# Performance work log

Hardware: AMD Instinct MI355X
Metric: run time of the kernel (lower is better)

## Reference

```python
import jax, jax.numpy as jnp
import numpy as np

B, S, P = 64, 32, 49
F, E, H, V = 2048, 512, 512, 32000


def setup_inputs() -> dict:
    key = jax.random.key(0)
    ks = jax.random.split(key, 20)
    sc = 0.02
    return {
        "captions": jax.random.randint(ks[0], (B, S), 0, V),
        "features": jax.random.normal(ks[1], (B, P, F), dtype=jnp.float32),
        "embed_table": jax.random.normal(ks[2], (V, E), dtype=jnp.float32) * sc,
        "W_a": jax.random.normal(ks[3], (H, F), dtype=jnp.float32) * sc,
        "b_Wa": jnp.zeros((H,), jnp.float32),
        "U_a": jax.random.normal(ks[4], (H, H), dtype=jnp.float32) * sc,
        "b_Ua": jnp.zeros((H,), jnp.float32),
        "v_a": jax.random.normal(ks[5], (1, H), dtype=jnp.float32) * sc,
        "b_va": jnp.zeros((1,), jnp.float32),
        "W_ih": jax.random.normal(ks[6], (4 * H, E + F), dtype=jnp.float32) * sc,
        "b_ih": jnp.zeros((4 * H,), jnp.float32),
        "W_hh": jax.random.normal(ks[7], (4 * H, H), dtype=jnp.float32) * sc,
        "b_hh": jnp.zeros((4 * H,), jnp.float32),
        "fc_W": jax.random.normal(ks[8], (V, H), dtype=jnp.float32) * sc,
        "fc_b": jnp.zeros((V,), jnp.float32),
        "Wh": jax.random.normal(ks[9], (H, F), dtype=jnp.float32) * sc,
        "bh": jnp.zeros((H,), jnp.float32),
        "Wc": jax.random.normal(ks[10], (H, F), dtype=jnp.float32) * sc,
        "bc": jnp.zeros((H,), jnp.float32),
    }


def reference(captions, features, embed_table, W_a, b_Wa, U_a, b_Ua, v_a, b_va,
              W_ih, b_ih, W_hh, b_hh, fc_W, fc_b, Wh, bh, Wc, bc):
    # Embedding lookup: [B, S, E]
    embed = embed_table[captions]
    # init hidden from mean annotation
    mean_feat = jnp.mean(features, axis=1)            # [B, F]
    h0 = mean_feat @ Wh.T + bh                        # [B, H]
    c0 = mean_feat @ Wc.T + bc
    # W_a(features) is time-invariant: precompute once
    att1 = jnp.einsum('bpf,hf->bph', features, W_a) + b_Wa  # [B, P, H]

    def step(carry, word_embed):
        h, c = carry
        # Bahdanau attention
        att2 = h @ U_a.T + b_Ua                                   # [B, H]
        score = jnp.tanh(att1 + att2[:, None, :]) @ v_a[0] + b_va[0]  # [B, P]
        w = jax.nn.softmax(score, axis=1)                         # [B, P]
        context = jnp.einsum('bp,bpf->bf', w, features)           # [B, F]
        # LSTMCell (PyTorch gate order: i, f, g, o)
        x = jnp.concatenate([word_embed, context], axis=1)        # [B, E+F]
        gates = x @ W_ih.T + b_ih + h @ W_hh.T + b_hh             # [B, 4H]
        i, f, g, o = jnp.split(gates, 4, axis=1)
        c_new = jax.nn.sigmoid(f) * c + jax.nn.sigmoid(i) * jnp.tanh(g)
        h_new = jax.nn.sigmoid(o) * jnp.tanh(c_new)
        # dropout is identity at inference
        logits = h_new @ fc_W.T + fc_b                            # [B, V]
        return (h_new, c_new), (logits, w)

    _, (logits, attw) = jax.lax.scan(step, (h0, c0), jnp.swapaxes(embed, 0, 1))
    outputs = jnp.swapaxes(logits, 0, 1)       # [B, S, V]
    atten_weights = jnp.swapaxes(attw, 0, 1)   # [B, S, P]
    return outputs, atten_weights
```

## Files before the change

kernel.cpp:

```cpp
#include <hip/hip_runtime.h>
#include <hip/hip_fp16.h>

typedef _Float16 f16;
typedef _Float16 f16x2 __attribute__((ext_vector_type(2)));
typedef _Float16 f16x4 __attribute__((ext_vector_type(4)));
typedef _Float16 f16x8 __attribute__((ext_vector_type(8)));
typedef float    f32x4 __attribute__((ext_vector_type(4)));


#define GLD16(g, l)                                                        \
  __builtin_amdgcn_global_load_lds(                                        \
      (const __attribute__((address_space(1))) void*)(g),                  \
      (__attribute__((address_space(3))) void*)(l), 16, 0, 0)

__global__ __launch_bounds__(256) void k_prep(
    const float* __restrict__ feat, const float* __restrict__ W_a,
    const float* __restrict__ W_ih, const float* __restrict__ fc_W,
    const float* __restrict__ W_hh, const float* __restrict__ U_a,
    const float* __restrict__ Wh, const float* __restrict__ Wc,
    const int* __restrict__ caps, const float* __restrict__ etab,
    f16* __restrict__ feat_h, f16* __restrict__ W_a_h,
    f16* __restrict__ W_ih_h, f16* __restrict__ fc_W_h,
    f16* __restrict__ Wcat_h, f16* __restrict__ Whc_h, f16* __restrict__ Aemb) {
  const long c0 = 1605632;
  const long c1 = c0 + 262144;
  const long c2 = c1 + 1310720;
  const long c3 = c2 + 4096000;
  const long c4 = c3 + 262144;
  const long c5 = c4 + 65536;
  const long c6 = c5 + 262144;
  const long c7 = c6 + 262144;
  const long c8 = c7 + 262144;
  long i = (long)blockIdx.x * 256 + threadIdx.x;
  const long stride = (long)gridDim.x * 256;
  for (; i < c8; i += stride) {
    const float4* s; f16x4* d; long j;
    if (i < c0)      { s = (const float4*)feat; d = (f16x4*)feat_h; j = i; }
    else if (i < c1) { s = (const float4*)W_a;  d = (f16x4*)W_a_h;  j = i - c0; }
    else if (i < c2) { s = (const float4*)W_ih; d = (f16x4*)W_ih_h; j = i - c1; }
    else if (i < c3) { s = (const float4*)fc_W; d = (f16x4*)fc_W_h; j = i - c2; }
    else if (i < c4) { s = (const float4*)W_hh; d = (f16x4*)Wcat_h; j = i - c3; }
    else if (i < c5) { s = (const float4*)U_a;  d = (f16x4*)(Wcat_h + 2048l * 512); j = i - c4; }
    else if (i < c6) { s = (const float4*)Wh;   d = (f16x4*)Whc_h;  j = i - c5; }
    else if (i < c7) { s = (const float4*)Wc;   d = (f16x4*)(Whc_h + 1048576l); j = i - c6; }
    else {
      long jj = i - c7;
      int n = (int)(jj >> 7), e4 = (int)(jj & 127);
      int tok = caps[n];
      s = (const float4*)(etab + (long)tok * 512); d = (f16x4*)(Aemb + (long)n * 512); j = e4;
    }
    float4 v = s[j];
    f16x4 o; o.x = (f16)v.x; o.y = (f16)v.y; o.z = (f16)v.z; o.w = (f16)v.w;
    d[j] = o;
  }
}

__global__ __launch_bounds__(256) void k_mean(const f16* __restrict__ feat_h,
                                              f16* __restrict__ mean_h) {
  int b = blockIdx.x;
  int e4 = blockIdx.y * 256 + threadIdx.x;
  const f16x4* src = (const f16x4*)(feat_h + (long)b * 49 * 2048) + e4;
  float s0 = 0.f, s1 = 0.f, s2 = 0.f, s3 = 0.f;
#pragma unroll 7
  for (int p = 0; p < 49; ++p) {
    f16x4 v = src[p * 512];
    s0 += (float)v.x; s1 += (float)v.y; s2 += (float)v.z; s3 += (float)v.w;
  }
  const float inv = 1.f / 49.f;
  f16x4 o; o.x = (f16)(s0 * inv); o.y = (f16)(s1 * inv); o.z = (f16)(s2 * inv); o.w = (f16)(s3 * inv);
  ((f16x4*)(mean_h + (long)b * 2048))[e4] = o;
}

__global__ __launch_bounds__(512) void k_h0split(const float* __restrict__ Rh0,
                                                 const float* __restrict__ bh,
                                                 const float* __restrict__ bc,
                                                 f16* __restrict__ h16,
                                                 float* __restrict__ c_state) {
  int b = blockIdx.x, j = threadIdx.x;
  h16[(long)b * 512 + j] = (f16)(Rh0[(long)b * 1024 + j] + bh[j]);
  c_state[(long)b * 512 + j] = Rh0[(long)b * 1024 + 512 + j] + bc[j];
}

__global__ __launch_bounds__(256) void k_gemm(const f16* __restrict__ A, long lda,
                                              const f16* __restrict__ Bw, long ldb,
                                              const float* __restrict__ bias1,
                                              const float* __restrict__ bias2,
                                              void* __restrict__ Cout, long ldc,
                                              int K, int mode, int n_mtiles) {
  __shared__ f16 As[64][40];
  __shared__ f16 Bs[64][40];
  const int tid = threadIdx.x;
  const int lane = tid & 63, wave = tid >> 6;
  const int bid = blockIdx.x;
  const long m0 = (long)(bid % n_mtiles) * 64, n0 = (long)(bid / n_mtiles) * 64;
  const int lr = tid >> 2, lc = (tid & 3) * 8;
  const int wr = (wave >> 1) * 32, wc = (wave & 1) * 32;
  f32x4 acc[2][2] = {};
  const f16* Ap = A + (m0 + lr) * lda + lc;
  const f16* Bp = Bw + (n0 + lr) * ldb + lc;
  for (int k0 = 0; k0 < K; k0 += 32) {
    uint4 av = *(const uint4*)(Ap + k0);
    uint4 bv = *(const uint4*)(Bp + k0);
    __syncthreads();
    *(uint4*)&As[lr][lc] = av;
    *(uint4*)&Bs[lr][lc] = bv;
    __syncthreads();
#pragma unroll
    for (int mi = 0; mi < 2; ++mi) {
      f16x8 af = *(const f16x8*)&As[wr + mi * 16 + (lane & 15)][(lane >> 4) * 8];
#pragma unroll
      for (int ni = 0; ni < 2; ++ni) {
        f16x8 bf = *(const f16x8*)&Bs[wc + ni * 16 + (lane & 15)][(lane >> 4) * 8];
        acc[mi][ni] = __builtin_amdgcn_mfma_f32_16x16x32_f16(af, bf, acc[mi][ni], 0, 0, 0);
      }
    }
  }
#pragma unroll
  for (int mi = 0; mi < 2; ++mi)
#pragma unroll
    for (int ni = 0; ni < 2; ++ni) {
      int row_b = wr + mi * 16 + (lane >> 4) * 4;
      long gcol = n0 + wc + ni * 16 + (lane & 15);
      float badd = (bias1 ? bias1[gcol] : 0.f) + (bias2 ? bias2[gcol] : 0.f);
#pragma unroll
      for (int r = 0; r < 4; ++r) {
        long grow = m0 + row_b + r;
        float v = acc[mi][ni][r] + badd;
        if (mode == 0)      ((float*)Cout)[grow * ldc + gcol] = v;
        else                ((f16*)Cout)[grow * ldc + gcol] = (f16)v;
      }
    }
}

__global__ __launch_bounds__(512) void k_gemm128b(const f16* __restrict__ A, long lda,
                                                  const f16* __restrict__ Bw, long ldb,
                                                  const float* __restrict__ bias1,
                                                  const float* __restrict__ bias2,
                                                  void* __restrict__ Cout, long ldc,
                                                  int K, int mode, int n_mtiles) {
  __shared__ f16 As[8192];
  __shared__ f16 Bs[8192];
  const int tid = threadIdx.x, lane = tid & 63, wave = tid >> 6;
  const int wm = wave & 3, wn = wave >> 2;
  const int bid = blockIdx.x;
  const long m0 = (long)(bid % n_mtiles) * 128, n0 = (long)(bid / n_mtiles) * 128;
  const int c0 = wave * 128 + lane, c1 = c0 + 64;
  const int r0 = c0 >> 3, s0 = (c0 & 7) ^ (r0 & 7);
  const int r1 = c1 >> 3, s1 = (c1 & 7) ^ (r1 & 7);
  const f16* gA0 = A + (m0 + r0) * lda + s0 * 8;
  const f16* gA1 = A + (m0 + r1) * lda + s1 * 8;
  const f16* gB0 = Bw + (n0 + r0) * ldb + s0 * 8;
  const f16* gB1 = Bw + (n0 + r1) * ldb + s1 * 8;
  f16* lA0 = As + (wave * 128) * 8;
  f16* lA1 = As + (wave * 128 + 64) * 8;
  f16* lB0 = Bs + (wave * 128) * 8;
  f16* lB1 = Bs + (wave * 128 + 64) * 8;
  f32x4 acc[2][4] = {};
  for (int k0 = 0; k0 < K; k0 += 64) {
    GLD16(gA0 + k0, lA0); GLD16(gA1 + k0, lA1);
    GLD16(gB0 + k0, lB0); GLD16(gB1 + k0, lB1);
    __syncthreads();
#pragma unroll
    for (int ks = 0; ks < 2; ++ks) {
      const int sp = (ks * 4 + (lane >> 4)) ^ (lane & 7);
#pragma unroll
      for (int mi = 0; mi < 2; ++mi) {
        const int rA = wm * 32 + mi * 16 + (lane & 15);
        f16x8 af = *(const f16x8*)(As + rA * 64 + sp * 8);
#pragma unroll
        for (int ni = 0; ni < 4; ++ni) {
          const int rB = wn * 64 + ni * 16 + (lane & 15);
          f16x8 bf = *(const f16x8*)(Bs + rB * 64 + sp * 8);
          acc[mi][ni] = __builtin_amdgcn_mfma_f32_16x16x32_f16(af, bf, acc[mi][ni], 0, 0, 0);
        }
      }
    }
    __syncthreads();
  }
#pragma unroll
  for (int mi = 0; mi < 2; ++mi)
#pragma unroll
    for (int ni = 0; ni < 4; ++ni) {
      int row_b = wm * 32 + mi * 16 + (lane >> 4) * 4;
      long gcol = n0 + wn * 64 + ni * 16 + (lane & 15);
      float badd = (bias1 ? bias1[gcol] : 0.f) + (bias2 ? bias2[gcol] : 0.f);
#pragma unroll
      for (int r = 0; r < 4; ++r) {
        long grow = m0 + row_b + r;
        float v = acc[mi][ni][r] + badd;
        if (mode == 0)      ((float*)Cout)[grow * ldc + gcol] = v;
        else if (mode == 1) ((f16*)Cout)[grow * ldc + gcol] = (f16)v;
        else                ((f16*)Cout)[grow * 2048 + ((gcol & 511) << 2) + (gcol >> 9)] = (f16)v;
      }
    }
}

__global__ __launch_bounds__(256) void k_rgemm(const f16* __restrict__ h16,
                                               const f16* __restrict__ Wcat,
                                               float* __restrict__ R) {
  const int tid = threadIdx.x, lane = tid & 63, wave = tid >> 6;
  const int n0 = blockIdx.x * 64;
  const int l15 = lane & 15;
  const int koff = (lane >> 4) * 8;
  f32x4 acc[4] = {};
  const f16* Ap = h16 + ((long)(wave * 16 + l15) << 9) + koff;
#pragma unroll
  for (int k0 = 0; k0 < 16; ++k0) {
    f16x8 af = *(const f16x8*)(Ap + k0 * 32);
#pragma unroll
    for (int ni = 0; ni < 4; ++ni) {
      f16x8 bf = *(const f16x8*)(Wcat + ((long)(n0 + ni * 16 + l15) << 9) + koff + k0 * 32);
      acc[ni] = __builtin_amdgcn_mfma_f32_16x16x32_f16(af, bf, acc[ni], 0, 0, 0);
    }
  }
  const int r0 = wave * 16 + (lane >> 4) * 4;
#pragma unroll
  for (int ni = 0; ni < 4; ++ni) {
    int col = n0 + ni * 16 + l15;
#pragma unroll
    for (int r = 0; r < 4; ++r)
      R[(long)(r0 + r) * 2560 + col] = acc[ni][r];
  }
}

__global__ __launch_bounds__(512) void k_step(const float* __restrict__ R,
                                              const float* __restrict__ b_Ua,
                                              const f16* __restrict__ att1,
                                              const float* __restrict__ va,
                                              const f16* __restrict__ featW4,
                                              const float* __restrict__ gates_x,
                                              float* __restrict__ c_state,
                                              f16* __restrict__ h16,
                                              f16* __restrict__ Hbuf,
                                              float* __restrict__ attw_out,
                                              int t) {
  __shared__ float att2[512];
  __shared__ float sc[64];
  __shared__ float wl[49];
  const int b = blockIdx.x, tid = threadIdx.x;
  const int lane = tid & 63, wave = tid >> 6;
  const long n = (long)b * 32 + t;
  const float* Rb = R + (long)b * 2560;
  const float* gx = gates_x + n * 2048;

  float g0 = gx[tid] + Rb[tid];
  float g1 = gx[512 + tid] + Rb[512 + tid];
  float g2 = gx[1024 + tid] + Rb[1024 + tid];
  float g3 = gx[1536 + tid] + Rb[1536 + tid];
  float c = c_state[(long)b * 512 + tid];

  att2[tid] = Rb[2048 + tid] + b_Ua[tid];
  __syncthreads();

  for (int p = wave; p < 49; p += 8) {
    const f16* arow = att1 + ((long)b * 49 + p) * 512;
    float s = 0.f;
#pragma unroll
    for (int kk = 0; kk < 8; ++kk) {
      int k = lane + kk * 64;
      float x = (float)arow[k] + att2[k];
      float e = __expf(2.f * x);
      float th = 1.f - 2.f / (e + 1.f);
      s += va[k] * th;
    }
#pragma unroll
    for (int off = 32; off; off >>= 1) s += __shfl_xor(s, off);
    if (lane == 0) sc[p] = s;
  }
  __syncthreads();

  if (wave == 0) {
    float s = (lane < 49) ? sc[lane] : -1e30f;
    float m = s;
#pragma unroll
    for (int off = 32; off; off >>= 1) m = fmaxf(m, __shfl_xor(m, off));
    float e = (lane < 49) ? __expf(s - m) : 0.f;
    float sum = e;
#pragma unroll
    for (int off = 32; off; off >>= 1) sum += __shfl_xor(sum, off);
    float wv = e / sum;
    if (lane < 49) { wl[lane] = wv; attw_out[n * 49 + lane] = wv; }
  }
  __syncthreads();

  const f16* fwbase = featW4 + (long)b * 49 * 2048 + tid * 4;
#pragma unroll
  for (int p = 0; p < 49; ++p) {
    float wp = wl[p];
    uint2 u = *(const uint2*)(fwbase + (long)p * 2048);
    f16x2 aa = __builtin_bit_cast(f16x2, u.x);
    f16x2 bb = __builtin_bit_cast(f16x2, u.y);
    g0 += wp * (float)aa.x; g1 += wp * (float)aa.y;
    g2 += wp * (float)bb.x; g3 += wp * (float)bb.y;
  }
  float iv = 1.f / (1.f + __expf(-g0));
  float fv = 1.f / (1.f + __expf(-g1));
  float e2 = __expf(2.f * g2); float gv = 1.f - 2.f / (e2 + 1.f);
  float ov = 1.f / (1.f + __expf(-g3));
  c = fv * c + iv * gv;
  float e3 = __expf(2.f * c); float tc = 1.f - 2.f / (e3 + 1.f);
  float hn = ov * tc;
  c_state[(long)b * 512 + tid] = c;
  h16[(long)b * 512 + tid] = (f16)hn;
  Hbuf[n * 512 + tid] = (f16)hn;
}

extern "C" void kernel_launch(void* const* d_in, const int* in_sizes, int n_in,
                              void* d_out, int out_size, void* d_ws, size_t ws_size,
                              hipStream_t stream) {
  const int*   caps = (const int*)d_in[0];
  const float* feat = (const float*)d_in[1];
  const float* etab = (const float*)d_in[2];
  const float* W_a  = (const float*)d_in[3];
  const float* b_Wa = (const float*)d_in[4];
  const float* U_a  = (const float*)d_in[5];
  const float* b_Ua = (const float*)d_in[6];
  const float* v_a  = (const float*)d_in[7];
  const float* W_ih = (const float*)d_in[9];
  const float* b_ih = (const float*)d_in[10];
  const float* W_hh = (const float*)d_in[11];
  const float* b_hh = (const float*)d_in[12];
  const float* fc_W = (const float*)d_in[13];
  const float* fc_b = (const float*)d_in[14];
  const float* Wh   = (const float*)d_in[15];
  const float* bh   = (const float*)d_in[16];
  const float* Wc   = (const float*)d_in[17];
  const float* bc   = (const float*)d_in[18];

  char* ws = (char*)d_ws;
  size_t off = 0;
  auto alloc = [&](size_t bytes) { void* p = ws + off; off += (bytes + 255) & ~(size_t)255; return p; };
  f16* feat_h  = (f16*)alloc(6553600ull * 2);
  f16* W_a_h   = (f16*)alloc(1048576ull * 2);
  f16* W_ih_h  = (f16*)alloc(5242880ull * 2);
  f16* fc_W_h  = (f16*)alloc(16384000ull * 2);
  f16* Aemb    = (f16*)alloc(1048576ull * 2);
  f16* Wcat_h  = (f16*)alloc(1310720ull * 2);
  f16* Whc_h   = (f16*)alloc(2097152ull * 2);
  f16* mean_h  = (f16*)alloc(131072ull * 2);
  f16* att1_h  = (f16*)alloc(1638400ull * 2);
  f16* featW4  = (f16*)alloc(6553600ull * 2);
  float* gates_x = (float*)alloc(4194304ull * 4);
  float* R     = (float*)alloc(163840ull * 4);
  f16* h16     = (f16*)alloc(32768ull * 2);
  float* c_state = (float*)alloc(32768ull * 4);
  f16* Hbuf    = (f16*)alloc(1048576ull * 2);
  (void)ws_size; (void)in_sizes; (void)n_in; (void)out_size;

  float* out_logits = (float*)d_out;
  float* out_attw   = out_logits + 65536000ull;

  k_prep<<<4096, 256, 0, stream>>>(feat, W_a, W_ih, fc_W, W_hh, U_a, Wh, Wc, caps, etab,
                                   feat_h, W_a_h, W_ih_h, fc_W_h, Wcat_h, Whc_h, Aemb);
  k_mean<<<dim3(64, 2), 256, 0, stream>>>(feat_h, mean_h);

  k_gemm<<<16, 256, 0, stream>>>(mean_h, 2048, Whc_h, 2048,
                                 nullptr, nullptr, R, 1024, 2048, 0, 1);
  k_h0split<<<64, 512, 0, stream>>>(R, bh, bc, h16, c_state);

  k_gemm128b<<<25 * 4, 512, 0, stream>>>(feat_h, 2048, W_a_h, 2048,
                                         b_Wa, nullptr, att1_h, 512, 2048, 1, 25);
  k_gemm128b<<<25 * 16, 512, 0, stream>>>(feat_h, 2048, W_ih_h + 512, 2560,
                                          nullptr, nullptr, featW4, 0, 2048, 2, 25);
  k_gemm128b<<<16 * 16, 512, 0, stream>>>(Aemb, 512, W_ih_h, 2560,
                                          b_ih, b_hh, gates_x, 2048, 512, 0, 16);

  for (int t = 0; t < 32; ++t) {
    k_rgemm<<<40, 256, 0, stream>>>(h16, Wcat_h, R);
    k_step<<<64, 512, 0, stream>>>(R, b_Ua, att1_h, v_a, featW4, gates_x,
                                   c_state, h16, Hbuf, out_attw, t);
  }

  k_gemm128b<<<16 * 250, 512, 0, stream>>>(Hbuf, 512, fc_W_h, 512,
                                           fc_b, nullptr, out_logits, 32000, 512, 0, 16);
}
```

Baseline: 983.4 us.

## Fuse recurrent GEMM into per-step kernel with split-hidden blocks and ping-pong state

The separate MFMA recurrent GEMM launch (h·[W_hh;U_a]) is removed. Its work moves into a single per-step kernel on a 64x4 grid, where each block owns 128 hidden units. W_hh is repacked into an interleaved [k/2][j][gate] fp16 layout so dot2 loads are coalesced. The U_a projection for the next step is computed as four partial sums from the new hidden slice and summed at the start of the next step, using ping-pong h/a2p buffers. This halves the launches per timestep. In exchange, the attention score and softmax are computed redundantly in all four blocks of each batch row, and the weight reads use scalar dot2 instead of MFMA.

Result: slower. 1.672 ms (+70.0%).

```diff
diff --git a/kernel.cpp b/kernel.cpp
--- a/kernel.cpp
+++ b/kernel.cpp
@@ -12,6 +12,14 @@
   __builtin_amdgcn_global_load_lds(                                        \
       (const __attribute__((address_space(1))) void*)(g),                  \
       (__attribute__((address_space(3))) void*)(l), 16, 0, 0)
+
+static __device__ __forceinline__ float fdot2f(f16x2 a, f16x2 b, float c) {
+#if __has_builtin(__builtin_amdgcn_fdot2)
+  return __builtin_amdgcn_fdot2(a, b, c, false);
+#else
+  return c + (float)a.x * (float)b.x + (float)a.y * (float)b.y;
+#endif
+}
 
 __global__ __launch_bounds__(256) void k_prep(
     const float* __restrict__ feat, const float* __restrict__ W_a,
@@ -21,7 +29,8 @@
     const int* __restrict__ caps, const float* __restrict__ etab,
     f16* __restrict__ feat_h, f16* __restrict__ W_a_h,
     f16* __restrict__ W_ih_h, f16* __restrict__ fc_W_h,
-    f16* __restrict__ Wcat_h, f16* __restrict__ Whc_h, f16* __restrict__ Aemb) {
+    f16* __restrict__ WhhP, f16* __restrict__ UaH,
+    f16* __restrict__ Whc_h, f16* __restrict__ Aemb) {
   const long c0 = 1605632;
   const long c1 = c0 + 262144;
   const long c2 = c1 + 1310720;
@@ -34,13 +43,25 @@
   long i = (long)blockIdx.x * 256 + threadIdx.x;
   const long stride = (long)gridDim.x * 256;
   for (; i < c8; i += stride) {
+    if (i >= c3 && i < c4) {
+      long ii = i - c3;
+      int row = (int)(ii >> 7);
+      int c4i = (int)(ii & 127);
+      int g = row >> 9, j = row & 511;
+      float4 v = ((const float4*)W_hh)[ii];
+      f16x2 p0; p0.x = (f16)v.x; p0.y = (f16)v.y;
+      f16x2 p1; p1.x = (f16)v.z; p1.y = (f16)v.w;
+      long k2a = 2 * (long)c4i;
+      ((f16x2*)WhhP)[k2a * 2048 + j * 4 + g] = p0;
+      ((f16x2*)WhhP)[(k2a + 1) * 2048 + j * 4 + g] = p1;
+      continue;
+    }
     const float4* s; f16x4* d; long j;
     if (i < c0)      { s = (const float4*)feat; d = (f16x4*)feat_h; j = i; }
     else if (i < c1) { s = (const float4*)W_a;  d = (f16x4*)W_a_h;  j = i - c0; }
     else if (i < c2) { s = (const float4*)W_ih; d = (f16x4*)W_ih_h; j = i - c1; }
     else if (i < c3) { s = (const float4*)fc_W; d = (f16x4*)fc_W_h; j = i - c2; }
-    else if (i < c4) { s = (const float4*)W_hh; d = (f16x4*)Wcat_h; j = i - c3; }
-    else if (i < c5) { s = (const float4*)U_a;  d = (f16x4*)(Wcat_h + 2048l * 512); j = i - c4; }
+    else if (i < c5) { s = (const float4*)U_a;  d = (f16x4*)UaH;    j = i - c4; }
     else if (i < c6) { s = (const float4*)Wh;   d = (f16x4*)Whc_h;  j = i - c5; }
     else if (i < c7) { s = (const float4*)Wc;   d = (f16x4*)(Whc_h + 1048576l); j = i - c6; }
     else {
@@ -71,22 +92,39 @@
   ((f16x4*)(mean_h + (long)b * 2048))[e4] = o;
 }
 
-__global__ __launch_bounds__(512) void k_h0split(const float* __restrict__ Rh0,
-                                                 const float* __restrict__ bh,
-                                                 const float* __restrict__ bc,
-                                                 f16* __restrict__ h16,
-                                                 float* __restrict__ c_state) {
-  int b = blockIdx.x, j = threadIdx.x;
-  h16[(long)b * 512 + j] = (f16)(Rh0[(long)b * 1024 + j] + bh[j]);
-  c_state[(long)b * 512 + j] = Rh0[(long)b * 1024 + 512 + j] + bc[j];
+__global__ __launch_bounds__(512) void k_h0a2p(const float* __restrict__ Rh0,
+                                               const float* __restrict__ bh,
+                                               const float* __restrict__ bc,
+                                               const f16* __restrict__ UaH,
+                                               f16* __restrict__ hA,
+                                               float* __restrict__ c_state,
+                                               float* __restrict__ a2pA) {
+  __shared__ f16 hsl[128];
+  const int b = blockIdx.x, q = blockIdx.y, tid = threadIdx.x;
+  if (tid < 128) {
+    int jg = q * 128 + tid;
+    float hv = Rh0[(long)b * 1024 + jg] + bh[jg];
+    c_state[(long)b * 512 + jg] = Rh0[(long)b * 1024 + 512 + jg] + bc[jg];
+    f16 hf = (f16)hv;
+    hsl[tid] = hf;
+    hA[(long)b * 512 + jg] = hf;
+  }
+  __syncthreads();
+  const f16x2* ua = (const f16x2*)(UaH + (long)tid * 512 + q * 128);
+  const f16x2* hv2 = (const f16x2*)hsl;
+  float s0 = 0.f, s1 = 0.f;
+#pragma unroll 8
+  for (int j2 = 0; j2 < 64; j2 += 2) {
+    s0 = fdot2f(hv2[j2], ua[j2], s0);
+    s1 = fdot2f(hv2[j2 + 1], ua[j2 + 1], s1);
+  }
+  a2pA[(long)b * 2048 + q * 512 + tid] = s0 + s1;
 }
 
 __global__ __launch_bounds__(256) void k_gemm(const f16* __restrict__ A, long lda,
                                               const f16* __restrict__ Bw, long ldb,
-                                              const float* __restrict__ bias1,
-                                              const float* __restrict__ bias2,
-                                              void* __restrict__ Cout, long ldc,
-                                              int K, int mode, int n_mtiles) {
+                                              float* __restrict__ Cout, long ldc,
+                                              int K, int n_mtiles) {
   __shared__ f16 As[64][40];
   __shared__ f16 Bs[64][40];
   const int tid = threadIdx.x;
@@ -121,14 +159,9 @@
     for (int ni = 0; ni < 2; ++ni) {
       int row_b = wr + mi * 16 + (lane >> 4) * 4;
       long gcol = n0 + wc + ni * 16 + (lane & 15);
-      float badd = (bias1 ? bias1[gcol] : 0.f) + (bias2 ? bias2[gcol] : 0.f);
-#pragma unroll
-      for (int r = 0; r < 4; ++r) {
-        long grow = m0 + row_b + r;
-        float v = acc[mi][ni][r] + badd;
-        if (mode == 0)      ((float*)Cout)[grow * ldc + gcol] = v;
-        else                ((f16*)Cout)[grow * ldc + gcol] = (f16)v;
-      }
+#pragma unroll
+      for (int r = 0; r < 4; ++r)
+        Cout[(m0 + row_b + r) * ldc + gcol] = acc[mi][ni][r];
     }
 }
 
@@ -195,61 +228,27 @@
     }
 }
 
-__global__ __launch_bounds__(256) void k_rgemm(const f16* __restrict__ h16,
-                                               const f16* __restrict__ Wcat,
-                                               float* __restrict__ R) {
-  const int tid = threadIdx.x, lane = tid & 63, wave = tid >> 6;
-  const int n0 = blockIdx.x * 64;
-  const int l15 = lane & 15;
-  const int koff = (lane >> 4) * 8;
-  f32x4 acc[4] = {};
-  const f16* Ap = h16 + ((long)(wave * 16 + l15) << 9) + koff;
-#pragma unroll
-  for (int k0 = 0; k0 < 16; ++k0) {
-    f16x8 af = *(const f16x8*)(Ap + k0 * 32);
-#pragma unroll
-    for (int ni = 0; ni < 4; ++ni) {
-      f16x8 bf = *(const f16x8*)(Wcat + ((long)(n0 + ni * 16 + l15) << 9) + koff + k0 * 32);
-      acc[ni] = __builtin_amdgcn_mfma_f32_16x16x32_f16(af, bf, acc[ni], 0, 0, 0);
-    }
-  }
-  const int r0 = wave * 16 + (lane >> 4) * 4;
-#pragma unroll
-  for (int ni = 0; ni < 4; ++ni) {
-    int col = n0 + ni * 16 + l15;
-#pragma unroll
-    for (int r = 0; r < 4; ++r)
-      R[(long)(r0 + r) * 2560 + col] = acc[ni][r];
-  }
-}
-
-__global__ __launch_bounds__(512) void k_step(const float* __restrict__ R,
-                                              const float* __restrict__ b_Ua,
-                                              const f16* __restrict__ att1,
-                                              const float* __restrict__ va,
-                                              const f16* __restrict__ featW4,
-                                              const float* __restrict__ gates_x,
-                                              float* __restrict__ c_state,
-                                              f16* __restrict__ h16,
-                                              f16* __restrict__ Hbuf,
-                                              float* __restrict__ attw_out,
-                                              int t) {
+__global__ __launch_bounds__(512) void k_fstep(
+    const f16* __restrict__ WhhP, const f16* __restrict__ UaH,
+    const float* __restrict__ b_Ua, const f16* __restrict__ att1,
+    const float* __restrict__ va, const f16* __restrict__ featW4,
+    const float* __restrict__ gates_x, float* __restrict__ c_state,
+    const f16* __restrict__ hin, f16* __restrict__ hout,
+    const float* __restrict__ a2pin, float* __restrict__ a2pout,
+    f16* __restrict__ Hbuf, float* __restrict__ attw_out, int t) {
+  __shared__ f16 hh[512];
   __shared__ float att2[512];
   __shared__ float sc[64];
   __shared__ float wl[49];
-  const int b = blockIdx.x, tid = threadIdx.x;
+  __shared__ float gl[128][5];
+  __shared__ f16 hsl[128];
+  const int b = blockIdx.x, q = blockIdx.y, tid = threadIdx.x;
   const int lane = tid & 63, wave = tid >> 6;
   const long n = (long)b * 32 + t;
-  const float* Rb = R + (long)b * 2560;
-  const float* gx = gates_x + n * 2048;
-
-  float g0 = gx[tid] + Rb[tid];
-  float g1 = gx[512 + tid] + Rb[512 + tid];
-  float g2 = gx[1024 + tid] + Rb[1024 + tid];
-  float g3 = gx[1536 + tid] + Rb[1536 + tid];
-  float c = c_state[(long)b * 512 + tid];
-
-  att2[tid] = Rb[2048 + tid] + b_Ua[tid];
+
+  hh[tid] = hin[(long)b * 512 + tid];
+  const float* ap = a2pin + (long)b * 2048;
+  att2[tid] = b_Ua[tid] + ap[tid] + ap[512 + tid] + ap[1024 + tid] + ap[1536 + tid];
   __syncthreads();
 
   for (int p = wave; p < 49; p += 8) {
@@ -260,8 +259,7 @@
       int k = lane + kk * 64;
       float x = (float)arow[k] + att2[k];
       float e = __expf(2.f * x);
-      float th = 1.f - 2.f / (e + 1.f);
-      s += va[k] * th;
+      s += va[k] * (1.f - 2.f / (e + 1.f));
     }
 #pragma unroll
     for (int off = 32; off; off >>= 1) s += __shfl_xor(s, off);
@@ -279,30 +277,67 @@
 #pragma unroll
     for (int off = 32; off; off >>= 1) sum += __shfl_xor(sum, off);
     float wv = e / sum;
-    if (lane < 49) { wl[lane] = wv; attw_out[n * 49 + lane] = wv; }
-  }
-  __syncthreads();
-
-  const f16* fwbase = featW4 + (long)b * 49 * 2048 + tid * 4;
-#pragma unroll
-  for (int p = 0; p < 49; ++p) {
-    float wp = wl[p];
-    uint2 u = *(const uint2*)(fwbase + (long)p * 2048);
-    f16x2 aa = __builtin_bit_cast(f16x2, u.x);
-    f16x2 bb = __builtin_bit_cast(f16x2, u.y);
-    g0 += wp * (float)aa.x; g1 += wp * (float)aa.y;
-    g2 += wp * (float)bb.x; g3 += wp * (float)bb.y;
-  }
-  float iv = 1.f / (1.f + __expf(-g0));
-  float fv = 1.f / (1.f + __expf(-g1));
-  float e2 = __expf(2.f * g2); float gv = 1.f - 2.f / (e2 + 1.f);
-  float ov = 1.f / (1.f + __expf(-g3));
-  c = fv * c + iv * gv;
-  float e3 = __expf(2.f * c); float tc = 1.f - 2.f / (e3 + 1.f);
-  float hn = ov * tc;
-  c_state[(long)b * 512 + tid] = c;
-  h16[(long)b * 512 + tid] = (f16)hn;
-  Hbuf[n * 512 + tid] = (f16)hn;
+    if (lane < 49) {
+      wl[lane] = wv;
+      if (q == 0) attw_out[n * 49 + lane] = wv;
+    }
+  }
+  __syncthreads();
+
+  const int jj = tid & 127, g = tid >> 7, jg = q * 128 + jj;
+  float gacc = gates_x[n * 2048 + g * 512 + jg];
+  {
+    const unsigned* wp = (const unsigned*)WhhP + jg * 4 + g;
+    const f16x2* hp = (const f16x2*)hh;
+    float a0 = 0.f, a1 = 0.f, a2 = 0.f, a3 = 0.f;
+#pragma unroll 8
+    for (int k2 = 0; k2 < 256; k2 += 4) {
+      a0 = fdot2f(hp[k2],     __builtin_bit_cast(f16x2, wp[(long)(k2) * 2048]),     a0);
+      a1 = fdot2f(hp[k2 + 1], __builtin_bit_cast(f16x2, wp[(long)(k2 + 1) * 2048]), a1);
+      a2 = fdot2f(hp[k2 + 2], __builtin_bit_cast(f16x2, wp[(long)(k2 + 2) * 2048]), a2);
+      a3 = fdot2f(hp[k2 + 3], __builtin_bit_cast(f16x2, wp[(long)(k2 + 3) * 2048]), a3);
+    }
+    gacc += (a0 + a1) + (a2 + a3);
+  }
+  {
+    const f16* fw = featW4 + (long)b * 49 * 2048 + jg * 4 + g;
+#pragma unroll 7
+    for (int p = 0; p < 49; ++p)
+      gacc += wl[p] * (float)fw[(long)p * 2048];
+  }
+  gl[jj][g] = gacc;
+  __syncthreads();
+
+  if (tid < 128) {
+    int jgl = q * 128 + tid;
+    float g0 = gl[tid][0], g1 = gl[tid][1], g2 = gl[tid][2], g3 = gl[tid][3];
+    float c = c_state[(long)b * 512 + jgl];
+    float iv = 1.f / (1.f + __expf(-g0));
+    float fv = 1.f / (1.f + __expf(-g1));
+    float e2 = __expf(2.f * g2); float gv = 1.f - 2.f / (e2 + 1.f);
+    float ov = 1.f / (1.f + __expf(-g3));
+    c = fv * c + iv * gv;
+    float e3 = __expf(2.f * c); float tc = 1.f - 2.f / (e3 + 1.f);
+    float hn = ov * tc;
+    c_state[(long)b * 512 + jgl] = c;
+    f16 hf = (f16)hn;
+    hsl[tid] = hf;
+    hout[(long)b * 512 + jgl] = hf;
+    Hbuf[n * 512 + jgl] = hf;
+  }
+  __syncthreads();
+
+  {
+    const f16x2* ua = (const f16x2*)(UaH + (long)tid * 512 + q * 128);
+    const f16x2* hv2 = (const f16x2*)hsl;
+    float s0 = 0.f, s1 = 0.f;
+#pragma unroll 8
+    for (int j2 = 0; j2 < 64; j2 += 2) {
+      s0 = fdot2f(hv2[j2], ua[j2], s0);
+      s1 = fdot2f(hv2[j2 + 1], ua[j2 + 1], s1);
+    }
+    a2pout[(long)b * 2048 + q * 512 + tid] = s0 + s1;
+  }
 }
 
 extern "C" void kernel_launch(void* const* d_in, const int* in_sizes, int n_in,
@@ -335,14 +370,18 @@
   f16* W_ih_h  = (f16*)alloc(5242880ull * 2);
   f16* fc_W_h  = (f16*)alloc(16384000ull * 2);
   f16* Aemb    = (f16*)alloc(1048576ull * 2);
-  f16* Wcat_h  = (f16*)alloc(1310720ull * 2);
+  f16* WhhP    = (f16*)alloc(1048576ull * 2);
+  f16* UaH     = (f16*)alloc(262144ull * 2);
   f16* Whc_h   = (f16*)alloc(2097152ull * 2);
   f16* mean_h  = (f16*)alloc(131072ull * 2);
   f16* att1_h  = (f16*)alloc(1638400ull * 2);
   f16* featW4  = (f16*)alloc(6553600ull * 2);
   float* gates_x = (float*)alloc(4194304ull * 4);
-  float* R     = (float*)alloc(163840ull * 4);
-  f16* h16     = (f16*)alloc(32768ull * 2);
+  float* Rh0   = (float*)alloc(65536ull * 4);
+  f16* hA      = (f16*)alloc(32768ull * 2);
+  f16* hB      = (f16*)alloc(32768ull * 2);
+  float* a2pA  = (float*)alloc(131072ull * 4);
+  float* a2pB  = (float*)alloc(131072ull * 4);
   float* c_state = (float*)alloc(32768ull * 4);
   f16* Hbuf    = (f16*)alloc(1048576ull * 2);
   (void)ws_size; (void)in_sizes; (void)n_in; (void)out_size;
@@ -351,12 +390,11 @@
   float* out_attw   = out_logits + 65536000ull;
 
   k_prep<<<4096, 256, 0, stream>>>(feat, W_a, W_ih, fc_W, W_hh, U_a, Wh, Wc, caps, etab,
-                                   feat_h, W_a_h, W_ih_h, fc_W_h, Wcat_h, Whc_h, Aemb);
+                                   feat_h, W_a_h, W_ih_h, fc_W_h, WhhP, UaH, Whc_h, Aemb);
   k_mean<<<dim3(64, 2), 256, 0, stream>>>(feat_h, mean_h);
 
-  k_gemm<<<16, 256, 0, stream>>>(mean_h, 2048, Whc_h, 2048,
-                                 nullptr, nullptr, R, 1024, 2048, 0, 1);
-  k_h0split<<<64, 512, 0, stream>>>(R, bh, bc, h16, c_state);
+  k_gemm<<<16, 256, 0, stream>>>(mean_h, 2048, Whc_h, 2048, Rh0, 1024, 2048, 1);
+  k_h0a2p<<<dim3(64, 4), 512, 0, stream>>>(Rh0, bh, bc, UaH, hA, c_state, a2pA);
 
   k_gemm128b<<<25 * 4, 512, 0, stream>>>(feat_h, 2048, W_a_h, 2048,
                                          b_Wa, nullptr, att1_h, 512, 2048, 1, 25);
@@ -366,9 +404,13 @@
                                           b_ih, b_hh, gates_x, 2048, 512, 0, 16);
 
   for (int t = 0; t < 32; ++t) {
-    k_rgemm<<<40, 256, 0, stream>>>(h16, Wcat_h, R);
-    k_step<<<64, 512, 0, stream>>>(R, b_Ua, att1_h, v_a, featW4, gates_x,
-                                   c_state, h16, Hbuf, out_attw, t);
+    const f16* hin = (t & 1) ? hB : hA;
+    f16* hout = (t & 1) ? hA : hB;
+    const float* a2i = (t & 1) ? a2pB : a2pA;
+    float* a2o = (t & 1) ? a2pA : a2pB;
+    k_fstep<<<dim3(64, 4), 512, 0, stream>>>(WhhP, UaH, b_Ua, att1_h, v_a, featW4,
+                                             gates_x, c_state, hin, hout, a2i, a2o,
+                                             Hbuf, out_attw, t);
   }
 
   k_gemm128b<<<16 * 250, 512, 0, stream>>>(Hbuf, 512, fc_W_h, 512,
```
